# Optimization experiments

Hardware: AMD Instinct MI355X
Metric: run time of the kernel (lower is better)

The kernel has to match this reference:

```python
import jax, jax.numpy as jnp
import numpy as np

B, S, W = 64, 128, 20
VOCAB, E, H = 256, 64, 256


def setup_inputs() -> dict:
    key = jax.random.key(0)
    ks = jax.random.split(key, 10)
    return {
        "chars": jax.random.randint(ks[0], (B, S, W), 0, VOCAB),
        "emb": jax.random.uniform(ks[1], (VOCAB, E), jnp.float32, -0.32, 0.32),
        "w1": jax.random.normal(ks[2], (H, E, 1), jnp.float32) * 0.1,
        "b1": jax.random.normal(ks[3], (H,), jnp.float32) * 0.1,
        "w3": jax.random.normal(ks[4], (H, E, 3), jnp.float32) * 0.1,
        "b3": jax.random.normal(ks[5], (H,), jnp.float32) * 0.1,
        "w5": jax.random.normal(ks[6], (H, E, 5), jnp.float32) * 0.1,
        "b5": jax.random.normal(ks[7], (H,), jnp.float32) * 0.1,
        "lw": jax.random.normal(ks[8], (H, 3 * H), jnp.float32) * 0.05,
        "lb": jax.random.normal(ks[9], (H,), jnp.float32) * 0.05,
    }


def _conv_relu_maxpool(x, w, b):
    # x: [N, E, W], w: [H, E, k] ('same' padding k//2) -> [N, H]
    k = w.shape[-1]
    pad = k // 2
    y = jax.lax.conv_general_dilated(
        x, w, window_strides=(1,), padding=[(pad, pad)],
        dimension_numbers=("NCH", "OIH", "NCH"))
    y = jax.nn.relu(y + b[None, :, None])
    return jnp.max(y, axis=2)  # global max over char positions


def reference(chars, emb, w1, b1, w3, b3, w5, b5, lw, lb):
    b, s, wlen = chars.shape
    flat = chars.reshape(-1, wlen)                 # [N, W]
    x = emb[flat]                                  # [N, W, E]
    x = jnp.transpose(x, (0, 2, 1))                # [N, E, W]
    outs = jnp.concatenate([
        _conv_relu_maxpool(x, w1, b1),
        _conv_relu_maxpool(x, w3, b3),
        _conv_relu_maxpool(x, w5, b5),
    ], axis=1)                                     # [N, 3H]
    out = outs @ lw.T + lb                         # [N, H]
    return out.reshape(b, s, -1)
```

## Files before the change

kernel.cpp:

```cpp
#include <hip/hip_runtime.h>
#include <hip/hip_bf16.h>

#define WW 20
#define NW 8192
#define VOCAB 256
#define EE 64
#define HH 256
#define K3 768
#define UNIT 2304

typedef short bf16x8 __attribute__((ext_vector_type(8)));
typedef float f32x4  __attribute__((ext_vector_type(4)));

__device__ __forceinline__ ushort f2bs(float x) {
    __hip_bfloat16 h = __float2bfloat16(x);
    union { __hip_bfloat16 h; ushort u; } c; c.h = h; return c.u;
}
__device__ __forceinline__ float blo(unsigned u) {
    union { unsigned i; float f; } c; c.i = u << 16; return c.f;
}
__device__ __forceinline__ float bhi(unsigned u) {
    union { unsigned i; float f; } c; c.i = u & 0xffff0000u; return c.f;
}
__device__ __forceinline__ unsigned pack2(float lo, float hi) {
    return (unsigned)f2bs(lo) | ((unsigned)f2bs(hi) << 16);
}

#define STEP(j, qq, t8v, a3, a5, mm1, mm3, mm5) {                        \
    float t0 = blo((qq).x), t1 = bhi((qq).x);                            \
    float t2 = blo((qq).y), t3 = bhi((qq).y);                            \
    float t4 = blo((qq).z), t5 = bhi((qq).z);                            \
    float t6 = blo((qq).w), t7 = bhi((qq).w);                            \
    mm1 = fmaxf(mm1, t0);                                                \
    if ((j) + 1 < WW) a3[((j)+1)%3] = t1;                                \
    a3[(j)%3] += t2;                                                     \
    if ((j) >= 1) { a3[((j)-1)%3] += t3;                                 \
                    mm3 = fmaxf(mm3, a3[((j)-1)%3]); }                   \
    if ((j) + 2 < WW) a5[((j)+2)%5] = t4;                                \
    if ((j) + 1 < WW) a5[((j)+1)%5] += t5;                               \
    a5[(j)%5] += t6;                                                     \
    if ((j) >= 1) a5[((j)-1)%5] += t7;                                   \
    if ((j) >= 2) { a5[((j)-2)%5] += (t8v);                              \
                    mm5 = fmaxf(mm5, a5[((j)-2)%5]); }                   \
}


__global__ __launch_bounds__(256) void prep(
        const float* __restrict__ w1,
        const float* __restrict__ w3,
        const float* __restrict__ w5,
        const float* __restrict__ lw,
        float* __restrict__ wTp,
        ushort* __restrict__ lwb) {
    const int bid = blockIdx.x;
    if (bid < 576) {
        int idx = bid * 256 + threadIdx.x;
        int e = idx / UNIT;
        int j = idx - e * UNIT;
        int s = j / 72, r = j - s * 72;
        int tap, h;
        if (r < 64) { tap = r & 7; h = s*8 + (r >> 3); }
        else        { tap = 8;     h = s*8 + (r - 64); }
        float v;
        if (tap == 0)      v = w1[h*EE + e];
        else if (tap <= 3) v = w3[(h*EE + e)*3 + (tap-1)];
        else               v = w5[(h*EE + e)*5 + (tap-4)];
        wTp[idx] = v;
    } else {
        int i = ((bid - 576) * 256 + threadIdx.x) * 4;
        float4 v = *(const float4*)(lw + i);
        ushort4 o4;
        o4.x = f2bs(v.x); o4.y = f2bs(v.y); o4.z = f2bs(v.z); o4.w = f2bs(v.w);
        *(ushort4*)(lwb + i) = o4;
    }
}

__global__ __launch_bounds__(256) void build_tables(
        const float* __restrict__ emb,
        const float* __restrict__ wTp,
        ushort* __restrict__ P5) {
    __shared__ float emb_s[4][EE];
    const int v0 = blockIdx.x * 4;
    const int j  = blockIdx.y * 256 + threadIdx.x;
    const int t  = threadIdx.x;
    emb_s[t >> 6][t & 63] = emb[v0*EE + t];
    __syncthreads();

    float a0 = 0.f, a1 = 0.f, a2 = 0.f, a3 = 0.f;
    const float* wp = wTp + j;
    #pragma unroll 8
    for (int e = 0; e < EE; ++e) {
        float w = wp[e * UNIT];
        a0 += emb_s[0][e] * w; a1 += emb_s[1][e] * w;
        a2 += emb_s[2][e] * w; a3 += emb_s[3][e] * w;
    }
    P5[(size_t)(v0+0)*UNIT + j] = f2bs(a0);
    P5[(size_t)(v0+1)*UNIT + j] = f2bs(a1);
    P5[(size_t)(v0+2)*UNIT + j] = f2bs(a2);
    P5[(size_t)(v0+3)*UNIT + j] = f2bs(a3);
}

__global__ __launch_bounds__(256) void conv_pool(
        const int* __restrict__ chars,
        const ushort* __restrict__ P5,
        const float* __restrict__ b1,
        const float* __restrict__ b3,
        const float* __restrict__ b5,
        ushort* __restrict__ outs) {
    __shared__ uint4 tileq[2304];
    const int t = threadIdx.x;
    const int g = blockIdx.x;
    const int s = blockIdx.y;

    {
        const char* src = (const char*)P5 + (size_t)s * 144;
        char* dst = (char*)tileq;
        #pragma unroll
        for (int i = 0; i < 9; ++i) {
            int c = i*256 + t;
            int v = c / 9, k = c - 9*v;
            *(uint4*)(dst + v*144 + k*16) =
                *(const uint4*)(src + (size_t)v*4608 + k*16);
        }
    }
    __syncthreads();

    const int p   = t & 3;
    const int wl0 = t >> 2;
    const char* tile = (const char*)tileq;
    const int h0  = s*8 + p*2;
    const float2 bb1 = *(const float2*)(b1 + h0);
    const float2 bb3 = *(const float2*)(b3 + h0);
    const float2 bb5 = *(const float2*)(b5 + h0);

    #pragma unroll
    for (int cc = 0; cc < 4; ++cc) {
        const int wl = cc*64 + wl0;
        const int n  = g*256 + wl;

        int cw[WW];
        {
            const int4* cp = (const int4*)(chars + n * WW);
            #pragma unroll
            for (int i = 0; i < 5; ++i) {
                int4 v = cp[i];
                cw[i*4+0] = v.x; cw[i*4+1] = v.y;
                cw[i*4+2] = v.z; cw[i*4+3] = v.w;
            }
        }

        float a3[2][3], a5[2][5], m1[2], m3[2], m5[2];
        #pragma unroll
        for (int i = 0; i < 2; ++i) {
            a3[i][0] = 0.f; a5[i][0] = 0.f; a5[i][1] = 0.f;
            m1[i] = -1e30f; m3[i] = -1e30f; m5[i] = -1e30f;
        }

        uint4 qa[2], qb[2]; unsigned t8[2];
        {
            int c0 = cw[0];
            qa[0] = *(const uint4*)(tile + c0*144 + p*32);
            qb[0] = *(const uint4*)(tile + c0*144 + p*32 + 16);
            t8[0] = *(const unsigned*)(tile + c0*144 + 128 + p*4);
        }

        #pragma unroll
        for (int j = 0; j < WW; ++j) {
            const int cur = j & 1, nxt = cur ^ 1;
            if (j + 1 < WW) {
                int cn = cw[j+1];
                qa[nxt] = *(const uint4*)(tile + cn*144 + p*32);
                qb[nxt] = *(const uint4*)(tile + cn*144 + p*32 + 16);
                t8[nxt] = *(const unsigned*)(tile + cn*144 + 128 + p*4);
            }
            float t8lo = blo(t8[cur]), t8hi = bhi(t8[cur]);
            STEP(j, qa[cur], t8lo, a3[0], a5[0], m1[0], m3[0], m5[0]);
            STEP(j, qb[cur], t8hi, a3[1], a5[1], m1[1], m3[1], m5[1]);
        }
        #pragma unroll
        for (int i = 0; i < 2; ++i) {
            m3[i] = fmaxf(m3[i], a3[i][(WW-1)%3]);
            m5[i] = fmaxf(m5[i], a5[i][(WW-2)%5]);
            m5[i] = fmaxf(m5[i], a5[i][(WW-1)%5]);
        }

        unsigned* op = (unsigned*)(outs + (size_t)n * K3 + h0);
        op[0*(HH/2)] = pack2(fmaxf(m1[0]+bb1.x, 0.f), fmaxf(m1[1]+bb1.y, 0.f));
        op[1*(HH/2)] = pack2(fmaxf(m3[0]+bb3.x, 0.f), fmaxf(m3[1]+bb3.y, 0.f));
        op[2*(HH/2)] = pack2(fmaxf(m5[0]+bb5.x, 0.f), fmaxf(m5[1]+bb5.y, 0.f));
    }
}

__global__ __launch_bounds__(64) void gemm_out(
        const ushort* __restrict__ outs,
        const ushort* __restrict__ lwb,
        const float* __restrict__ lb,
        float* __restrict__ out) {
    const int lane = threadIdx.x;
    const int m0 = blockIdx.x * 32;
    const int n0 = blockIdx.y * 32;
    const int mrow = lane & 15, quad = lane >> 4;

    f32x4 acc00 = (f32x4){0,0,0,0}, acc01 = (f32x4){0,0,0,0};
    f32x4 acc10 = (f32x4){0,0,0,0}, acc11 = (f32x4){0,0,0,0};
    const ushort* ap = outs + (size_t)(m0 + mrow) * K3 + quad * 8;
    const ushort* bp = lwb  + (size_t)(n0 + mrow) * K3 + quad * 8;

    bf16x8 a0 = *(const bf16x8*)ap, a1 = *(const bf16x8*)(ap + 16*K3);
    bf16x8 b0 = *(const bf16x8*)bp, b1 = *(const bf16x8*)(bp + 16*K3);

    #pragma unroll
    for (int it = 0; it < K3/32; ++it) {
        const int kn = (it + 1 < K3/32) ? (it + 1) * 32 : 0;
        bf16x8 a0n = *(const bf16x8*)(ap + kn);
        bf16x8 a1n = *(const bf16x8*)(ap + 16*K3 + kn);
        bf16x8 b0n = *(const bf16x8*)(bp + kn);
        bf16x8 b1n = *(const bf16x8*)(bp + 16*K3 + kn);
        acc00 = __builtin_amdgcn_mfma_f32_16x16x32_bf16(a0, b0, acc00, 0, 0, 0);
        acc01 = __builtin_amdgcn_mfma_f32_16x16x32_bf16(a0, b1, acc01, 0, 0, 0);
        acc10 = __builtin_amdgcn_mfma_f32_16x16x32_bf16(a1, b0, acc10, 0, 0, 0);
        acc11 = __builtin_amdgcn_mfma_f32_16x16x32_bf16(a1, b1, acc11, 0, 0, 0);
        a0 = a0n; a1 = a1n; b0 = b0n; b1 = b1n;
    }

    #pragma unroll
    for (int i = 0; i < 2; ++i) {
        #pragma unroll
        for (int jn = 0; jn < 2; ++jn) {
            const f32x4 acc = (i==0) ? (jn==0 ? acc00 : acc01)
                                     : (jn==0 ? acc10 : acc11);
            int ncol = n0 + jn*16 + mrow;
            float lbv = lb[ncol];
            #pragma unroll
            for (int r = 0; r < 4; ++r)
                out[(size_t)(m0 + i*16 + quad*4 + r)*HH + ncol] = acc[r] + lbv;
        }
    }
}

extern "C" void kernel_launch(void* const* d_in, const int* in_sizes, int n_in,
                              void* d_out, int out_size, void* d_ws, size_t ws_size,
                              hipStream_t stream) {
    const int*   chars = (const int*)d_in[0];
    const float* emb   = (const float*)d_in[1];
    const float* w1    = (const float*)d_in[2];
    const float* b1    = (const float*)d_in[3];
    const float* w3    = (const float*)d_in[4];
    const float* b3    = (const float*)d_in[5];
    const float* w5    = (const float*)d_in[6];
    const float* b5    = (const float*)d_in[7];
    const float* lw    = (const float*)d_in[8];
    const float* lb    = (const float*)d_in[9];

    ushort* P5   = (ushort*)d_ws;
    float*  wTp  = (float*)(P5 + VOCAB * UNIT);
    ushort* outs = (ushort*)(wTp + EE * UNIT);
    ushort* lwb  = outs + (size_t)NW * K3;

    prep<<<768, 256, 0, stream>>>(w1, w3, w5, lw, wTp, lwb);
    build_tables<<<dim3(VOCAB/4, 9), 256, 0, stream>>>(emb, wTp, P5);
    conv_pool<<<dim3(NW/256, 32), 256, 0, stream>>>(chars, P5, b1, b3, b5, outs);
    gemm_out<<<dim3(NW/32, HH/32), 64, 0, stream>>>(outs, lwb, lb, (float*)d_out);
}
```

Baseline: 130.5 us.

## Fuse weight prep into table build and deepen GEMM operand prefetch

The separate prep kernel is removed. build_tables now gathers the conv weights straight from w1/w3/w5 into registers, and an extra grid row converts lw to bf16. This drops one launch and the wTp round trip through global memory, but the weight reads are now strided and uncoalesced. Separately, gemm_out's register prefetch of A/B fragments goes from one K-step ahead to three, using 4-slot register rings, which raises register pressure.

```diff
diff --git a/kernel.cpp b/kernel.cpp
--- a/kernel.cpp
+++ b/kernel.cpp
@@ -45,54 +45,56 @@
 }
 
 
-__global__ __launch_bounds__(256) void prep(
+__global__ __launch_bounds__(256) void build_tables(
+        const float* __restrict__ emb,
         const float* __restrict__ w1,
         const float* __restrict__ w3,
         const float* __restrict__ w5,
         const float* __restrict__ lw,
-        float* __restrict__ wTp,
+        ushort* __restrict__ P5,
         ushort* __restrict__ lwb) {
-    const int bid = blockIdx.x;
-    if (bid < 576) {
-        int idx = bid * 256 + threadIdx.x;
-        int e = idx / UNIT;
-        int j = idx - e * UNIT;
-        int s = j / 72, r = j - s * 72;
-        int tap, h;
-        if (r < 64) { tap = r & 7; h = s*8 + (r >> 3); }
-        else        { tap = 8;     h = s*8 + (r - 64); }
-        float v;
-        if (tap == 0)      v = w1[h*EE + e];
-        else if (tap <= 3) v = w3[(h*EE + e)*3 + (tap-1)];
-        else               v = w5[(h*EE + e)*5 + (tap-4)];
-        wTp[idx] = v;
-    } else {
-        int i = ((bid - 576) * 256 + threadIdx.x) * 4;
-        float4 v = *(const float4*)(lw + i);
-        ushort4 o4;
-        o4.x = f2bs(v.x); o4.y = f2bs(v.y); o4.z = f2bs(v.z); o4.w = f2bs(v.w);
-        *(ushort4*)(lwb + i) = o4;
-    }
-}
-
-__global__ __launch_bounds__(256) void build_tables(
-        const float* __restrict__ emb,
-        const float* __restrict__ wTp,
-        ushort* __restrict__ P5) {
-    __shared__ float emb_s[4][EE];
+    __shared__ __align__(16) float emb_s[EE][4];
+    const int t = threadIdx.x;
+
+    if (blockIdx.y == 9) {
+        int i0 = (blockIdx.x * 256 + t) * 4;
+        #pragma unroll
+        for (int rr = 0; rr < 3; ++rr) {
+            int i = i0 + rr * 65536;
+            float4 v = *(const float4*)(lw + i);
+            ushort4 o4;
+            o4.x = f2bs(v.x); o4.y = f2bs(v.y);
+            o4.z = f2bs(v.z); o4.w = f2bs(v.w);
+            *(ushort4*)(lwb + i) = o4;
+        }
+        return;
+    }
+
     const int v0 = blockIdx.x * 4;
-    const int j  = blockIdx.y * 256 + threadIdx.x;
-    const int t  = threadIdx.x;
-    emb_s[t >> 6][t & 63] = emb[v0*EE + t];
+    const int j  = blockIdx.y * 256 + t;
+
+    emb_s[t & 63][t >> 6] = emb[v0 * EE + t];
+
+    const int s = j / 72, r = j - s * 72;
+    int tap, h;
+    if (r < 64) { tap = r & 7; h = s*8 + (r >> 3); }
+    else        { tap = 8;     h = s*8 + (r - 64); }
+    const float* wp; int st;
+    if (tap == 0)      { wp = w1 + h*EE;                 st = 1; }
+    else if (tap <= 3) { wp = w3 + (h*EE)*3 + (tap-1);   st = 3; }
+    else               { wp = w5 + (h*EE)*5 + (tap-4);   st = 5; }
+    float wreg[EE];
+    #pragma unroll
+    for (int e = 0; e < EE; ++e) wreg[e] = wp[e * st];
+
     __syncthreads();
 
     float a0 = 0.f, a1 = 0.f, a2 = 0.f, a3 = 0.f;
-    const float* wp = wTp + j;
-    #pragma unroll 8
+    #pragma unroll
     for (int e = 0; e < EE; ++e) {
-        float w = wp[e * UNIT];
-        a0 += emb_s[0][e] * w; a1 += emb_s[1][e] * w;
-        a2 += emb_s[2][e] * w; a3 += emb_s[3][e] * w;
+        const float4 ev = *(const float4*)(&emb_s[e][0]);
+        a0 += ev.x * wreg[e]; a1 += ev.y * wreg[e];
+        a2 += ev.z * wreg[e]; a3 += ev.w * wreg[e];
     }
     P5[(size_t)(v0+0)*UNIT + j] = f2bs(a0);
     P5[(size_t)(v0+1)*UNIT + j] = f2bs(a1);
@@ -206,21 +208,28 @@
     const ushort* ap = outs + (size_t)(m0 + mrow) * K3 + quad * 8;
     const ushort* bp = lwb  + (size_t)(n0 + mrow) * K3 + quad * 8;
 
-    bf16x8 a0 = *(const bf16x8*)ap, a1 = *(const bf16x8*)(ap + 16*K3);
-    bf16x8 b0 = *(const bf16x8*)bp, b1 = *(const bf16x8*)(bp + 16*K3);
+    bf16x8 A0[4], A1[4], B0[4], B1[4];
+    #pragma unroll
+    for (int pi = 0; pi < 3; ++pi) {
+        A0[pi] = *(const bf16x8*)(ap + pi*32);
+        A1[pi] = *(const bf16x8*)(ap + 16*K3 + pi*32);
+        B0[pi] = *(const bf16x8*)(bp + pi*32);
+        B1[pi] = *(const bf16x8*)(bp + 16*K3 + pi*32);
+    }
 
     #pragma unroll
     for (int it = 0; it < K3/32; ++it) {
-        const int kn = (it + 1 < K3/32) ? (it + 1) * 32 : 0;
-        bf16x8 a0n = *(const bf16x8*)(ap + kn);
-        bf16x8 a1n = *(const bf16x8*)(ap + 16*K3 + kn);
-        bf16x8 b0n = *(const bf16x8*)(bp + kn);
-        bf16x8 b1n = *(const bf16x8*)(bp + 16*K3 + kn);
-        acc00 = __builtin_amdgcn_mfma_f32_16x16x32_bf16(a0, b0, acc00, 0, 0, 0);
-        acc01 = __builtin_amdgcn_mfma_f32_16x16x32_bf16(a0, b1, acc01, 0, 0, 0);
-        acc10 = __builtin_amdgcn_mfma_f32_16x16x32_bf16(a1, b0, acc10, 0, 0, 0);
-        acc11 = __builtin_amdgcn_mfma_f32_16x16x32_bf16(a1, b1, acc11, 0, 0, 0);
-        a0 = a0n; a1 = a1n; b0 = b0n; b1 = b1n;
+        const int sl = it & 3;
+        const int nl = (it + 3) & 3;
+        const int kn = (it + 3 < K3/32) ? (it + 3) * 32 : 0;
+        A0[nl] = *(const bf16x8*)(ap + kn);
+        A1[nl] = *(const bf16x8*)(ap + 16*K3 + kn);
+        B0[nl] = *(const bf16x8*)(bp + kn);
+        B1[nl] = *(const bf16x8*)(bp + 16*K3 + kn);
+        acc00 = __builtin_amdgcn_mfma_f32_16x16x32_bf16(A0[sl], B0[sl], acc00, 0, 0, 0);
+        acc01 = __builtin_amdgcn_mfma_f32_16x16x32_bf16(A0[sl], B1[sl], acc01, 0, 0, 0);
+        acc10 = __builtin_amdgcn_mfma_f32_16x16x32_bf16(A1[sl], B0[sl], acc10, 0, 0, 0);
+        acc11 = __builtin_amdgcn_mfma_f32_16x16x32_bf16(A1[sl], B1[sl], acc11, 0, 0, 0);
     }
 
     #pragma unroll
@@ -253,12 +262,10 @@
     const float* lb    = (const float*)d_in[9];
 
     ushort* P5   = (ushort*)d_ws;
-    float*  wTp  = (float*)(P5 + VOCAB * UNIT);
-    ushort* outs = (ushort*)(wTp + EE * UNIT);
+    ushort* outs = P5 + (size_t)VOCAB * UNIT;
     ushort* lwb  = outs + (size_t)NW * K3;
 
-    prep<<<768, 256, 0, stream>>>(w1, w3, w5, lw, wTp, lwb);
-    build_tables<<<dim3(VOCAB/4, 9), 256, 0, stream>>>(emb, wTp, P5);
+    build_tables<<<dim3(VOCAB/4, 10), 256, 0, stream>>>(emb, w1, w3, w5, lw, P5, lwb);
     conv_pool<<<dim3(NW/256, 32), 256, 0, stream>>>(chars, P5, b1, b3, b5, outs);
     gemm_out<<<dim3(NW/32, HH/32), 64, 0, stream>>>(outs, lwb, lb, (float*)d_out);
 }
```

Measured after the change: 137.1 us. 1.05x slower.
